# Kernel tuning notes

Measured on AMD Instinct MI355X. Metric: run time of the kernel, lower is better.

The kernel has to match this reference:

```python
import jax, jax.numpy as jnp
import numpy as np

B, T, I, H, O = 65536, 28, 28, 64, 10


def setup_inputs() -> dict:
    key = jax.random.key(0)
    ks = jax.random.split(key, 8)
    s = 1.0 / np.sqrt(H)
    return {
        "x": jax.random.normal(ks[0], (B, T, I), dtype=jnp.float32),
        # PyTorch LSTM params: gate order i, f, g, o stacked along first dim
        "W_ih": jax.random.uniform(ks[1], (4 * H, I), minval=-s, maxval=s, dtype=jnp.float32),
        "W_hh": jax.random.uniform(ks[2], (4 * H, H), minval=-s, maxval=s, dtype=jnp.float32),
        "b_ih": jax.random.uniform(ks[3], (4 * H,), minval=-s, maxval=s, dtype=jnp.float32),
        "b_hh": jax.random.uniform(ks[4], (4 * H,), minval=-s, maxval=s, dtype=jnp.float32),
        "W_out": jax.random.uniform(ks[5], (O, H), minval=-s, maxval=s, dtype=jnp.float32),
        "b_out": jax.random.uniform(ks[6], (O,), minval=-s, maxval=s, dtype=jnp.float32),
    }


def _lstm_last_h(x, W_ih, W_hh, b_ih, b_hh):
    # x: [B, T, I]; returns final hidden state h_T: [B, H]
    b = b_ih + b_hh
    # precompute input projections for all timesteps: [T, B, 4H]
    xg = jnp.einsum("bti,gi->tbg", x, W_ih) + b

    def step(carry, xg_t):
        h, c = carry
        gates = xg_t + h @ W_hh.T  # [B, 4H]
        i, f, g, o = jnp.split(gates, 4, axis=-1)
        i = jax.nn.sigmoid(i)
        f = jax.nn.sigmoid(f)
        g = jnp.tanh(g)
        o = jax.nn.sigmoid(o)
        c = f * c + i * g
        h = o * jnp.tanh(c)
        return (h, c), None

    h0 = jnp.zeros((x.shape[0], W_hh.shape[1]), dtype=x.dtype)
    (h, c), _ = jax.lax.scan(step, (h0, h0), xg)
    return h


def reference(x, W_ih, W_hh, b_ih, b_hh, W_out, b_out):
    h = _lstm_last_h(x, W_ih, W_hh, b_ih, b_hh)  # [B, H]
    return h @ W_out.T + b_out  # [B, O]
```

## Files before the change

kernel.cpp:

```cpp
#include <hip/hip_runtime.h>
#include <hip/hip_bf16.h>
#include <stdint.h>
#include <stddef.h>

#define T_STEPS 28
#define I_DIM 28
#define H_DIM 64
#define O_DIM 10
#define BT 64
#define NTHREADS 512

typedef short bf16x8  __attribute__((ext_vector_type(8)));
typedef float f32x4   __attribute__((ext_vector_type(4)));

#define KS (-1.4426950408889634f)
#define KG ( 2.8853900817779268f)

__device__ __forceinline__ short f2bf(float f){
    uint32_t u = __builtin_bit_cast(uint32_t, f);
    u = (u + 0x7fffu + ((u >> 16) & 1u)) >> 16;
    return (short)u;
}
__device__ __forceinline__ float bf2f(short v){
    return __builtin_bit_cast(float, (uint32_t)(uint16_t)v << 16);
}
__device__ __forceinline__ uint32_t pack_bf16x2(float lo, float hi){
    float2 p2; p2.x = lo; p2.y = hi;
    __hip_bfloat162 p = __float22bfloat162_rn(p2);
    uint32_t u;
    __builtin_memcpy(&u, &p, 4);
    return u;
}

#define X_OFF(b)  ((b) * 5120)
#define H_OFF(b)  (10240 + (b) * 9216)
#define SMEM_BYTES (31232 + 48)

__global__ __launch_bounds__(NTHREADS, 4)
void lstm_fused(const float* __restrict__ x,
                const float* __restrict__ W_ih,
                const float* __restrict__ W_hh,
                const float* __restrict__ b_ih,
                const float* __restrict__ b_hh,
                const float* __restrict__ W_out,
                const float* __restrict__ b_out,
                float* __restrict__ out)
{
    __shared__ alignas(16) unsigned char smem[SMEM_BYTES];
    float* wout_t = (float*)(smem + 28672);
    float* bout_s = (float*)(smem + 31232);

    const int tid    = threadIdx.x;
    const int w      = tid >> 6;
    const int jgroup = w & 3;
    const int mgroup = w >> 2;
    const int lane = tid & 63;
    const int col  = lane & 15;
    const int quad = lane >> 4;
    const int jcol = jgroup * 16 + col;
    const int b0   = blockIdx.x * BT;

    bf16x8 wih[4];
    bf16x8 whh[2][4];
    f32x4  bias4[4];
    #pragma unroll
    for (int nt = 0; nt < 4; ++nt){
        const float sc = (nt == 2) ? KG : KS;
        const int n = nt * 64 + jgroup * 16 + col;
        #pragma unroll
        for (int j = 0; j < 8; ++j){
            const int k = quad * 8 + j;
            wih[nt][j] = (k < I_DIM) ? f2bf(sc * W_ih[n * I_DIM + k]) : (short)0;
        }
        #pragma unroll
        for (int s = 0; s < 2; ++s)
            #pragma unroll
            for (int j = 0; j < 8; ++j){
                const int k = s * 32 + quad * 8 + j;
                whh[s][nt][j] = f2bf(sc * W_hh[n * H_DIM + k]);
            }
        const float b = sc * (b_ih[n] + b_hh[n]);
        f32x4 bv; bv[0] = b; bv[1] = b; bv[2] = b; bv[3] = b;
        bias4[nt] = bv;
    }

    for (int idx = tid; idx < H_DIM * O_DIM; idx += NTHREADS){
        const int j = idx / O_DIM;
        const int o = idx - j * O_DIM;
        wout_t[idx] = W_out[o * H_DIM + j];
    }
    if (tid < O_DIM) bout_s[tid] = b_out[tid];

    for (int idx = tid; idx < 64 * 72; idx += NTHREADS)
        ((short*)(smem + H_OFF(0)))[idx] = 0;

    const int row = tid >> 3;
    const int seg = tid & 7;
    const float* pxs = x + (size_t)(b0 + row) * (T_STEPS * I_DIM) + seg * 4;

    float xa[4];
    #pragma unroll
    for (int u = 0; u < 4; ++u)
        xa[u] = (seg * 4 + u < I_DIM) ? pxs[u] : 0.0f;
    pxs += I_DIM;

    float cst[2][4];
    #pragma unroll
    for (int m = 0; m < 2; ++m)
        #pragma unroll
        for (int r = 0; r < 4; ++r) cst[m][r] = 0.0f;

    for (int t = 0; t < T_STEPS; ++t){
        short (*xb)[40] = (short(*)[40])(smem + X_OFF(t & 1));
        {
            uint2 v;
            v.x = pack_bf16x2(xa[0], xa[1]);
            v.y = pack_bf16x2(xa[2], xa[3]);
            *(uint2*)&xb[row][seg * 4] = v;
        }
        __syncthreads();

        if (t < T_STEPS - 1){
            #pragma unroll
            for (int u = 0; u < 4; ++u)
                if (seg * 4 + u < I_DIM) xa[u] = pxs[u];
            pxs += I_DIM;
        }

        const short (*hr)[72] = (const short(*)[72])(smem + H_OFF(t & 1));
        short (*hw)[72]       = (short(*)[72])(smem + H_OFF((t + 1) & 1));

        #pragma unroll
        for (int m = 0; m < 2; ++m){
            const int mt = mgroup * 2 + m;

            f32x4 acc[4];
            {
                bf16x8 a = *(const bf16x8*)&xb[mt * 16 + col][quad * 8];
                #pragma unroll
                for (int nt = 0; nt < 4; ++nt)
                    acc[nt] = __builtin_amdgcn_mfma_f32_16x16x32_bf16(a, wih[nt], bias4[nt], 0, 0, 0);
            }
            #pragma unroll
            for (int s = 0; s < 2; ++s){
                bf16x8 a = *(const bf16x8*)&hr[mt * 16 + col][s * 32 + quad * 8];
                #pragma unroll
                for (int nt = 0; nt < 4; ++nt)
                    acc[nt] = __builtin_amdgcn_mfma_f32_16x16x32_bf16(a, whh[s][nt], acc[nt], 0, 0, 0);
            }

            float hv[4];
            #pragma unroll
            for (int r = 0; r < 4; ++r){
                const float gi = __builtin_amdgcn_rcpf(1.0f + __builtin_amdgcn_exp2f(acc[0][r]));
                const float gf = __builtin_amdgcn_rcpf(1.0f + __builtin_amdgcn_exp2f(acc[1][r]));
                const float rg = __builtin_amdgcn_rcpf(1.0f + __builtin_amdgcn_exp2f(acc[2][r]));
                const float gg = 1.0f - 2.0f * rg;
                const float go = __builtin_amdgcn_rcpf(1.0f + __builtin_amdgcn_exp2f(acc[3][r]));
                const float c_ = gf * cst[m][r] + gi * gg;
                cst[m][r] = c_;
                const float rc = __builtin_amdgcn_rcpf(1.0f + __builtin_amdgcn_exp2f(KG * c_));
                hv[r] = go * (1.0f - 2.0f * rc);
            }
            #pragma unroll
            for (int rp = 0; rp < 2; ++rp){
                uint32_t u = pack_bf16x2(hv[2 * rp], hv[2 * rp + 1]);
                hw[mt * 16 + quad * 4 + 2 * rp    ][jcol] = (short)(u & 0xffffu);
                hw[mt * 16 + quad * 4 + 2 * rp + 1][jcol] = (short)(u >> 16);
            }
        }
    }
    __syncthreads();

    const short (*hfin)[72] = (const short(*)[72])(smem + H_OFF(0));
    for (int idx = tid; idx < BT * O_DIM; idx += NTHREADS){
        const int m = idx / O_DIM;
        const int o = idx - m * O_DIM;
        float s = bout_s[o];
        #pragma unroll 8
        for (int j = 0; j < H_DIM; ++j)
            s += bf2f(hfin[m][j]) * wout_t[j * O_DIM + o];
        out[(size_t)b0 * O_DIM + idx] = s;
    }
}

extern "C" void kernel_launch(void* const* d_in, const int* in_sizes, int n_in,
                              void* d_out, int out_size, void* d_ws, size_t ws_size,
                              hipStream_t stream) {
    const float* x     = (const float*)d_in[0];
    const float* W_ih  = (const float*)d_in[1];
    const float* W_hh  = (const float*)d_in[2];
    const float* b_ih  = (const float*)d_in[3];
    const float* b_hh  = (const float*)d_in[4];
    const float* W_out = (const float*)d_in[5];
    const float* b_out = (const float*)d_in[6];
    float* out = (float*)d_out;

    const int grid = 65536 / BT;
    lstm_fused<<<grid, NTHREADS, 0, stream>>>(x, W_ih, W_hh, b_ih, b_hh, W_out, b_out, out);
}
```

Measured before the change: 381.1 us.

## Halve block size, fold bias into MFMA, share reciprocals across gate pairs

Shrinks each block to 32 batch rows and 4 waves so blocks are smaller and more numerous. It folds the combined bias into the padded K slot of the input-projection MFMA by feeding a constant 1.0 input column, which frees the bias registers. It also merges pairs of reciprocals into one reciprocal of the product, cutting transcendental rcp ops by about half. In exchange the bias is rounded to bf16, and the product of two denominators could overflow to inf for large pre-activations, which may give NaN or loss of accuracy.

```diff
diff --git a/kernel.cpp b/kernel.cpp
--- a/kernel.cpp
+++ b/kernel.cpp
@@ -7,8 +7,8 @@
 #define I_DIM 28
 #define H_DIM 64
 #define O_DIM 10
-#define BT 64
-#define NTHREADS 512
+#define BT 32
+#define NTHREADS 256
 
 typedef short bf16x8  __attribute__((ext_vector_type(8)));
 typedef float f32x4   __attribute__((ext_vector_type(4)));
@@ -32,9 +32,9 @@
     return u;
 }
 
-#define X_OFF(b)  ((b) * 5120)
-#define H_OFF(b)  (10240 + (b) * 9216)
-#define SMEM_BYTES (31232 + 48)
+#define X_OFF(b)  ((b) * 2560)
+#define H_OFF(b)  (5120 + (b) * 4608)
+#define SMEM_BYTES (16896 + 48)
 
 __global__ __launch_bounds__(NTHREADS, 4)
 void lstm_fused(const float* __restrict__ x,
@@ -47,13 +47,12 @@
                 float* __restrict__ out)
 {
     __shared__ alignas(16) unsigned char smem[SMEM_BYTES];
-    float* wout_t = (float*)(smem + 28672);
-    float* bout_s = (float*)(smem + 31232);
+    float* wout_t = (float*)(smem + 14336);
+    float* bout_s = (float*)(smem + 16896);
 
     const int tid    = threadIdx.x;
     const int w      = tid >> 6;
-    const int jgroup = w & 3;
-    const int mgroup = w >> 2;
+    const int jgroup = w;
     const int lane = tid & 63;
     const int col  = lane & 15;
     const int quad = lane >> 4;
@@ -62,7 +61,6 @@
 
     bf16x8 wih[4];
     bf16x8 whh[2][4];
-    f32x4  bias4[4];
     #pragma unroll
     for (int nt = 0; nt < 4; ++nt){
         const float sc = (nt == 2) ? KG : KS;
@@ -70,7 +68,9 @@
         #pragma unroll
         for (int j = 0; j < 8; ++j){
             const int k = quad * 8 + j;
-            wih[nt][j] = (k < I_DIM) ? f2bf(sc * W_ih[n * I_DIM + k]) : (short)0;
+            wih[nt][j] = (k < I_DIM) ? f2bf(sc * W_ih[n * I_DIM + k])
+                       : (k == I_DIM) ? f2bf(sc * (b_ih[n] + b_hh[n]))
+                       : (short)0;
         }
         #pragma unroll
         for (int s = 0; s < 2; ++s)
@@ -79,10 +79,8 @@
                 const int k = s * 32 + quad * 8 + j;
                 whh[s][nt][j] = f2bf(sc * W_hh[n * H_DIM + k]);
             }
-        const float b = sc * (b_ih[n] + b_hh[n]);
-        f32x4 bv; bv[0] = b; bv[1] = b; bv[2] = b; bv[3] = b;
-        bias4[nt] = bv;
-    }
+    }
+    const f32x4 z4 = {0.0f, 0.0f, 0.0f, 0.0f};
 
     for (int idx = tid; idx < H_DIM * O_DIM; idx += NTHREADS){
         const int j = idx / O_DIM;
@@ -91,7 +89,7 @@
     }
     if (tid < O_DIM) bout_s[tid] = b_out[tid];
 
-    for (int idx = tid; idx < 64 * 72; idx += NTHREADS)
+    for (int idx = tid; idx < BT * 72; idx += NTHREADS)
         ((short*)(smem + H_OFF(0)))[idx] = 0;
 
     const int row = tid >> 3;
@@ -100,8 +98,10 @@
 
     float xa[4];
     #pragma unroll
-    for (int u = 0; u < 4; ++u)
-        xa[u] = (seg * 4 + u < I_DIM) ? pxs[u] : 0.0f;
+    for (int u = 0; u < 4; ++u){
+        const int c = seg * 4 + u;
+        xa[u] = (c < I_DIM) ? pxs[u] : (c == I_DIM ? 1.0f : 0.0f);
+    }
     pxs += I_DIM;
 
     float cst[2][4];
@@ -132,14 +132,14 @@
 
         #pragma unroll
         for (int m = 0; m < 2; ++m){
-            const int mt = mgroup * 2 + m;
+            const int mt = m;
 
             f32x4 acc[4];
             {
                 bf16x8 a = *(const bf16x8*)&xb[mt * 16 + col][quad * 8];
                 #pragma unroll
                 for (int nt = 0; nt < 4; ++nt)
-                    acc[nt] = __builtin_amdgcn_mfma_f32_16x16x32_bf16(a, wih[nt], bias4[nt], 0, 0, 0);
+                    acc[nt] = __builtin_amdgcn_mfma_f32_16x16x32_bf16(a, wih[nt], z4, 0, 0, 0);
             }
             #pragma unroll
             for (int s = 0; s < 2; ++s){
@@ -151,16 +151,34 @@
 
             float hv[4];
             #pragma unroll
-            for (int r = 0; r < 4; ++r){
-                const float gi = __builtin_amdgcn_rcpf(1.0f + __builtin_amdgcn_exp2f(acc[0][r]));
-                const float gf = __builtin_amdgcn_rcpf(1.0f + __builtin_amdgcn_exp2f(acc[1][r]));
-                const float rg = __builtin_amdgcn_rcpf(1.0f + __builtin_amdgcn_exp2f(acc[2][r]));
-                const float gg = 1.0f - 2.0f * rg;
-                const float go = __builtin_amdgcn_rcpf(1.0f + __builtin_amdgcn_exp2f(acc[3][r]));
-                const float c_ = gf * cst[m][r] + gi * gg;
-                cst[m][r] = c_;
-                const float rc = __builtin_amdgcn_rcpf(1.0f + __builtin_amdgcn_exp2f(KG * c_));
-                hv[r] = go * (1.0f - 2.0f * rc);
+            for (int p = 0; p < 2; ++p){
+                const int r0 = 2 * p, r1 = 2 * p + 1;
+                const float dA0 = 1.0f + __builtin_amdgcn_exp2f(acc[0][r0]);
+                const float dA1 = 1.0f + __builtin_amdgcn_exp2f(acc[0][r1]);
+                const float dB0 = 1.0f + __builtin_amdgcn_exp2f(acc[1][r0]);
+                const float dB1 = 1.0f + __builtin_amdgcn_exp2f(acc[1][r1]);
+                const float R10 = __builtin_amdgcn_rcpf(dA0 * dB0);
+                const float R11 = __builtin_amdgcn_rcpf(dA1 * dB1);
+                const float iv0 = R10 * dB0, fv0 = R10 * dA0;
+                const float iv1 = R11 * dB1, fv1 = R11 * dA1;
+                const float dG0 = 1.0f + __builtin_amdgcn_exp2f(acc[2][r0]);
+                const float dG1 = 1.0f + __builtin_amdgcn_exp2f(acc[2][r1]);
+                const float dO0 = 1.0f + __builtin_amdgcn_exp2f(acc[3][r0]);
+                const float dO1 = 1.0f + __builtin_amdgcn_exp2f(acc[3][r1]);
+                const float R20 = __builtin_amdgcn_rcpf(dG0 * dO0);
+                const float R21 = __builtin_amdgcn_rcpf(dG1 * dO1);
+                const float ov0 = R20 * dG0, ov1 = R21 * dG1;
+                const float gv0 = 1.0f - 2.0f * (R20 * dO0);
+                const float gv1 = 1.0f - 2.0f * (R21 * dO1);
+                const float c0 = fv0 * cst[m][r0] + iv0 * gv0;
+                const float c1 = fv1 * cst[m][r1] + iv1 * gv1;
+                cst[m][r0] = c0; cst[m][r1] = c1;
+                const float d50 = 1.0f + __builtin_amdgcn_exp2f(KG * c0);
+                const float d51 = 1.0f + __builtin_amdgcn_exp2f(KG * c1);
+                const float R5 = __builtin_amdgcn_rcpf(d50 * d51);
+                const float t2 = 2.0f * R5;
+                hv[r0] = ov0 * (1.0f - t2 * d51);
+                hv[r1] = ov1 * (1.0f - t2 * d50);
             }
             #pragma unroll
             for (int rp = 0; rp < 2; ++rp){
```

New measurement: 373.3 us. -2.1%, faster.
